# Performance work log

Measured on AMD Instinct MI355X. Metric: run time of the kernel, lower is better.

Reference implementation:

```python
import jax, jax.numpy as jnp
import numpy as np

B = 1024            # batch of input bit patterns
T = 1024            # total_input_bits
N = 2048            # num_neurons
NB = 16             # n_bits_per_neuron
M = 1 << NB         # memory_size = 65536
TRUE_VAL = 1        # MemoryVal.TRUE (0=FALSE, 1=TRUE, 2=EMPTY)


def setup_inputs() -> dict:
    key = jax.random.key(0)
    k1, k2, k3 = jax.random.split(key, 3)
    input_bits = jax.random.randint(k1, (B, T), 0, 2, dtype=jnp.int32)
    connections = jax.random.randint(k2, (N, NB), 0, T, dtype=jnp.int32)
    # dense representation of the sparse dict: codes 0/1/2 (FALSE/TRUE/EMPTY)
    memory_table = jax.random.randint(k3, (N, M), 0, 3).astype(jnp.float32)
    return {"input_bits": input_bits, "connections": connections,
            "memory_table": memory_table}


def reference(input_bits, connections, memory_table):
    # binarize input (any nonzero -> 1), as in get_addresses
    bits = (input_bits != 0).astype(jnp.int32)            # [B, T]
    # per-neuron gather of connected input bits
    gathered = bits[:, connections]                        # [B, N, NB]
    # MSB-first binary weights: 2^(NB-1) ... 2^0
    weights = (1 << jnp.arange(NB - 1, -1, -1)).astype(jnp.int32)  # [NB]
    addresses = (gathered * weights).sum(-1)               # [B, N] in [0, M)
    # sparse cell read: memory_table[n, addr] for each (b, n)
    rows = jnp.arange(N)[None, :]                          # [1, N]
    mem_vals = memory_table[rows, addresses]               # [B, N]
    # forward: TRUE cells -> True, FALSE/EMPTY -> False
    return mem_vals == jnp.float32(TRUE_VAL)
```

## Files before the change

### kernel.cpp

```cpp
#include <hip/hip_runtime.h>
#include <stdint.h>

#define BB 1024
#define TT 1024
#define NN 2048
#define NBITS 16
#define MM 65536
#define BW (BB/64)

__global__ void pack_transpose_kernel(const int* __restrict__ in,
                                      unsigned long long* __restrict__ bitsT) {
    const int lane = threadIdx.x & 63;
    const int wave = threadIdx.x >> 6;
    const int w  = blockIdx.y;
    const int t0 = blockIdx.x * 64 + wave * 16;
    const int b  = w * 64 + lane;
    const int* row = in + (size_t)b * TT;
    #pragma unroll
    for (int i = 0; i < 16; ++i) {
        const int t = t0 + i;
        const int v = row[t];
        unsigned long long m = __ballot(v != 0);
        if (lane == 0) bitsT[(size_t)t * BW + w] = m;
    }
}

__global__ void lookup_kernel(const int* __restrict__ conn,
                              const float* __restrict__ table,
                              const unsigned long long* __restrict__ bitsT,
                              int* __restrict__ out) {
    const int tn = threadIdx.x & 15;
    const int s  = threadIdx.x >> 4;
    const int n  = blockIdx.x * 16 + tn;
    const int b0 = blockIdx.y * 256 + s * 16;

    int tk[NBITS];
    #pragma unroll
    for (int k = 0; k < NBITS; ++k) tk[k] = conn[n * NBITS + k];

    unsigned int hw[NBITS];
    {
        const int w  = b0 >> 6;
        const int jb = b0 & 63;
        #pragma unroll
        for (int k = 0; k < NBITS; ++k) {
            unsigned long long word = bitsT[(size_t)tk[k] * BW + w];
            hw[k] = (unsigned int)(word >> jb) & 0xFFFFu;
        }
    }

    const float* trow = table + (size_t)n * MM;
    #pragma unroll
    for (int j = 0; j < 16; ++j) {
        unsigned int addr = 0;
        #pragma unroll
        for (int k = 0; k < NBITS; ++k) {
            addr |= ((hw[k] >> j) & 1u) << (NBITS - 1 - k);
        }
        const float v = trow[addr];
        out[(size_t)(b0 + j) * NN + n] = (v == 1.0f) ? 1 : 0;
    }
}

extern "C" void kernel_launch(void* const* d_in, const int* in_sizes, int n_in,
                              void* d_out, int out_size, void* d_ws, size_t ws_size,
                              hipStream_t stream) {
    const int*   in_bits = (const int*)d_in[0];
    const int*   conn    = (const int*)d_in[1];
    const float* table   = (const float*)d_in[2];
    int* out = (int*)d_out;

    unsigned long long* bitsT = (unsigned long long*)d_ws;

    dim3 g1(TT / 64, BB / 64);
    pack_transpose_kernel<<<g1, 256, 0, stream>>>(in_bits, bitsT);

    dim3 g2(NN / 16, BB / 256);
    lookup_kernel<<<g2, 256, 0, stream>>>(conn, table, bitsT, out);
}
```

Baseline: 50.47 us.

## Sort per-neuron lookup addresses by bucket and bit-pack results before expanding

Gives each neuron its own block. The block computes the neuron's 1024 addresses, counting-sorts them by address bucket in shared memory, and then gathers from the table row in sorted order so that nearby lanes hit nearby cache lines. Results are packed into a bit-transposed workspace and expanded to the int output by a separate coalesced kernel that uses nontemporal stores. This replaces strided scattered gathers and strided output writes, at the cost of an extra kernel launch, shared-memory atomics and several block barriers. The old path is kept as a fallback when the workspace is too small.

```diff
diff --git a/kernel.cpp b/kernel.cpp
--- a/kernel.cpp
+++ b/kernel.cpp
@@ -6,7 +6,7 @@
 #define NN 2048
 #define NBITS 16
 #define MM 65536
-#define BW (BB/64)
+#define BW 16
 
 __global__ void pack_transpose_kernel(const int* __restrict__ in,
                                       unsigned long long* __restrict__ bitsT) {
@@ -25,40 +25,127 @@
     }
 }
 
-__global__ void lookup_kernel(const int* __restrict__ conn,
-                              const float* __restrict__ table,
-                              const unsigned long long* __restrict__ bitsT,
+__global__ __launch_bounds__(256) void sorted_gather_kernel(
+        const int* __restrict__ conn,
+        const float* __restrict__ table,
+        const unsigned long long* __restrict__ bitsT,
+        unsigned long long* __restrict__ resbitsT) {
+    __shared__ unsigned long long sb[NBITS * BW];
+    __shared__ unsigned int hist[64];
+    __shared__ unsigned int cursor[64];
+    __shared__ unsigned int sorted[BB];
+    __shared__ unsigned char resb[BB];
+
+    const int tid = threadIdx.x;
+    const int n   = blockIdx.x;
+
+    {
+        const int k = tid >> 4;
+        const int w = tid & 15;
+        const int t = conn[n * NBITS + k];
+        sb[k * BW + w] = bitsT[(size_t)t * BW + w];
+    }
+    if (tid < 64) hist[tid] = 0;
+    __syncthreads();
+
+    const int wi = tid >> 4;
+    unsigned long long wreg[NBITS];
+    #pragma unroll
+    for (int k = 0; k < NBITS; ++k) wreg[k] = sb[k * BW + wi];
+
+    unsigned int addr[4];
+    #pragma unroll
+    for (int j = 0; j < 4; ++j) {
+        const int bit = (4 * tid + j) & 63;
+        unsigned int a = 0;
+        #pragma unroll
+        for (int k = 0; k < NBITS; ++k)
+            a |= (unsigned int)((wreg[k] >> bit) & 1ull) << (NBITS - 1 - k);
+        addr[j] = a;
+        atomicAdd(&hist[a >> 10], 1u);
+    }
+    __syncthreads();
+
+    if (tid < 64) {
+        const unsigned int v = hist[tid];
+        unsigned int s = v;
+        #pragma unroll
+        for (int d = 1; d < 64; d <<= 1) {
+            const unsigned int t2 = (unsigned int)__shfl_up((int)s, d, 64);
+            if (tid >= d) s += t2;
+        }
+        cursor[tid] = s - v;
+    }
+    __syncthreads();
+
+    #pragma unroll
+    for (int j = 0; j < 4; ++j) {
+        const unsigned int a   = addr[j];
+        const unsigned int pos = atomicAdd(&cursor[a >> 10], 1u);
+        sorted[pos] = (a << 16) | (unsigned int)(4 * tid + j);
+    }
+    __syncthreads();
+
+    const int lane = tid & 63;
+    const int wv   = tid >> 6;
+    const float* trow = table + (size_t)n * MM;
+    unsigned int it[4];
+    float v[4];
+    #pragma unroll
+    for (int j = 0; j < 4; ++j) it[j] = sorted[wv * 256 + j * 64 + lane];
+    #pragma unroll
+    for (int j = 0; j < 4; ++j) v[j] = trow[it[j] >> 16];
+    #pragma unroll
+    for (int j = 0; j < 4; ++j)
+        resb[it[j] & 0xFFFFu] = (v[j] == 1.0f) ? 1 : 0;
+    __syncthreads();
+
+    #pragma unroll
+    for (int w4 = 0; w4 < 4; ++w4) {
+        const int w = wv * 4 + w4;
+        const unsigned long long m = __ballot(resb[w * 64 + lane] != 0);
+        if (lane == 0) resbitsT[(size_t)w * NN + n] = m;
+    }
+}
+
+__global__ void expand_kernel(const unsigned long long* __restrict__ resbitsT,
                               int* __restrict__ out) {
+    const int idx = blockIdx.x * 256 + threadIdx.x;
+    const int n = idx & (NN - 1);
+    const int b = idx >> 11;
+    const unsigned long long w = resbitsT[(size_t)(b >> 6) * NN + n];
+    const int r = (int)((w >> (b & 63)) & 1ull);
+    __builtin_nontemporal_store(r, &out[idx]);
+}
+
+__global__ __launch_bounds__(256) void lookup_direct_kernel(
+        const int* __restrict__ conn,
+        const float* __restrict__ table,
+        const unsigned long long* __restrict__ bitsT,
+        int* __restrict__ out) {
     const int tn = threadIdx.x & 15;
     const int s  = threadIdx.x >> 4;
     const int n  = blockIdx.x * 16 + tn;
     const int b0 = blockIdx.y * 256 + s * 16;
-
     int tk[NBITS];
     #pragma unroll
     for (int k = 0; k < NBITS; ++k) tk[k] = conn[n * NBITS + k];
-
     unsigned int hw[NBITS];
-    {
-        const int w  = b0 >> 6;
-        const int jb = b0 & 63;
-        #pragma unroll
-        for (int k = 0; k < NBITS; ++k) {
-            unsigned long long word = bitsT[(size_t)tk[k] * BW + w];
-            hw[k] = (unsigned int)(word >> jb) & 0xFFFFu;
-        }
+    const int w  = b0 >> 6;
+    const int jb = b0 & 63;
+    #pragma unroll
+    for (int k = 0; k < NBITS; ++k) {
+        unsigned long long word = bitsT[(size_t)tk[k] * BW + w];
+        hw[k] = (unsigned int)(word >> jb) & 0xFFFFu;
     }
-
     const float* trow = table + (size_t)n * MM;
     #pragma unroll
     for (int j = 0; j < 16; ++j) {
-        unsigned int addr = 0;
+        unsigned int a = 0;
         #pragma unroll
-        for (int k = 0; k < NBITS; ++k) {
-            addr |= ((hw[k] >> j) & 1u) << (NBITS - 1 - k);
-        }
-        const float v = trow[addr];
-        out[(size_t)(b0 + j) * NN + n] = (v == 1.0f) ? 1 : 0;
+        for (int k = 0; k < NBITS; ++k)
+            a |= ((hw[k] >> j) & 1u) << (NBITS - 1 - k);
+        out[(size_t)(b0 + j) * NN + n] = (trow[a] == 1.0f) ? 1 : 0;
     }
 }
 
@@ -70,11 +157,19 @@
     const float* table   = (const float*)d_in[2];
     int* out = (int*)d_out;
 
-    unsigned long long* bitsT = (unsigned long long*)d_ws;
+    const size_t bitsT_bytes = (size_t)TT * BW * 8;
+    const size_t res_bytes   = (size_t)BW * NN * 8;
+    unsigned long long* bitsT    = (unsigned long long*)d_ws;
+    unsigned long long* resbitsT = (unsigned long long*)((char*)d_ws + bitsT_bytes);
 
     dim3 g1(TT / 64, BB / 64);
     pack_transpose_kernel<<<g1, 256, 0, stream>>>(in_bits, bitsT);
 
-    dim3 g2(NN / 16, BB / 256);
-    lookup_kernel<<<g2, 256, 0, stream>>>(conn, table, bitsT, out);
+    if (ws_size >= bitsT_bytes + res_bytes) {
+        sorted_gather_kernel<<<NN, 256, 0, stream>>>(conn, table, bitsT, resbitsT);
+        expand_kernel<<<(BB * NN) / 256, 256, 0, stream>>>(resbitsT, out);
+    } else {
+        dim3 g2(NN / 16, BB / 256);
+        lookup_direct_kernel<<<g2, 256, 0, stream>>>(conn, table, bitsT, out);
+    }
 }
```

After: 46.35 us, median of 2. 1.09x faster.
